# Kernel optimization log

Hardware: AMD Instinct MI355X
Metric: run time of the kernel (lower is better)

The kernel has to match this reference:

```python
import jax, jax.numpy as jnp
import numpy as np

EMBED_DIM = 1024
NUM_HEADS = 16
HEAD_DIM = EMBED_DIM // NUM_HEADS


def setup_inputs() -> dict:
    key = jax.random.key(0)
    ks = jax.random.split(key, 5)
    B, N, C = 2, 2048, EMBED_DIM
    s = 0.02
    return {
        "x": jax.random.normal(ks[0], (B, N, C), dtype=jnp.float32),
        "w_qkv": jax.random.normal(ks[1], (C, 3 * C), dtype=jnp.float32) * s,
        "b_qkv": jax.random.normal(ks[2], (3 * C,), dtype=jnp.float32) * s,
        "w_proj": jax.random.normal(ks[3], (C, C), dtype=jnp.float32) * s,
        "b_proj": jax.random.normal(ks[4], (C,), dtype=jnp.float32) * s,
    }


def reference(x, w_qkv, b_qkv, w_proj, b_proj):
    B, N, C = x.shape
    H, D = NUM_HEADS, C // NUM_HEADS
    scale = D ** -0.5
    qkv = x @ w_qkv + b_qkv                      # [B,N,3C]
    qkv = qkv.reshape(B, N, 3, H, D).transpose(2, 0, 3, 1, 4)  # [3,B,H,N,D]
    q, k, v = qkv[0] * scale, qkv[1], qkv[2]
    attn = jnp.einsum("bhnd,bhmd->bhnm", q, k)   # [B,H,N,N]
    attn = jax.nn.softmax(attn, axis=-1)
    out = jnp.einsum("bhnm,bhmd->bhnd", attn, v)  # [B,H,N,D]
    out = out.transpose(0, 2, 1, 3).reshape(B, N, C)
    return out @ w_proj + b_proj
```

## Files before the change

### kernel.cpp

```cpp
#include <hip/hip_runtime.h>

typedef short bf16x8 __attribute__((ext_vector_type(8)));
typedef float f32x4 __attribute__((ext_vector_type(4)));
typedef float f32x16 __attribute__((ext_vector_type(16)));
typedef unsigned short ushort8 __attribute__((ext_vector_type(8)));
typedef unsigned short ushort4v __attribute__((ext_vector_type(4)));
typedef unsigned int uint4v __attribute__((ext_vector_type(4)));
typedef unsigned short u16;

__device__ inline u16 f2bf(float f) {
  unsigned int u = __float_as_uint(f);
  u += 0x7fffu + ((u >> 16) & 1u);
  return (u16)(u >> 16);
}

__device__ inline unsigned cvt_pk_bf16(float lo, float hi2) {
  unsigned r;
  asm("v_cvt_pk_bf16_f32 %0, %1, %2" : "=v"(r) : "v"(lo), "v"(hi2));
  return r;
}

__device__ inline void perm32swap(unsigned& a, unsigned& b) {
  asm("v_permlane32_swap_b32 %0, %1" : "+v"(a), "+v"(b));
}

__device__ inline void gload_lds16(const u16* g, u16* l) {
  __builtin_amdgcn_global_load_lds(
      (const __attribute__((address_space(1))) unsigned int*)g,
      (__attribute__((address_space(3))) unsigned int*)l, 16, 0, 0);
}

__global__ __launch_bounds__(256) void cvt_bf16(const float* __restrict__ in,
                                                u16* __restrict__ out, int n) {
  int i = (blockIdx.x * 256 + threadIdx.x) * 8;
  if (i >= n) return;
  float4 a = *(const float4*)(in + i);
  float4 b = *(const float4*)(in + i + 4);
  ushort8 o;
  o[0] = f2bf(a.x); o[1] = f2bf(a.y); o[2] = f2bf(a.z); o[3] = f2bf(a.w);
  o[4] = f2bf(b.x); o[5] = f2bf(b.y); o[6] = f2bf(b.z); o[7] = f2bf(b.w);
  *(ushort8*)(out + i) = o;
}

__global__ __launch_bounds__(256) void trans_w(const float* __restrict__ W,
                                               u16* __restrict__ Wt, int K, int N) {
  const int k0 = blockIdx.x * 64, n0 = blockIdx.y * 64;
  const int tx = threadIdx.x & 63, ty = threadIdx.x >> 6;
  __shared__ float t[64][65];
#pragma unroll
  for (int i = 0; i < 16; ++i) {
    int r = i * 4 + ty;
    t[r][tx] = W[(size_t)(k0 + r) * N + n0 + tx];
  }
  __syncthreads();
#pragma unroll
  for (int i = 0; i < 16; ++i) {
    int r = i * 4 + ty;
    Wt[(size_t)(n0 + r) * K + k0 + tx] = f2bf(t[tx][r]);
  }
}

template <int MODE>
__global__ __launch_bounds__(256) void gemm_bt(
    const u16* __restrict__ A, const u16* __restrict__ Bt, int M, int N, int K,
    const float* __restrict__ bias, float* __restrict__ outF,
    u16* __restrict__ Qb, u16* __restrict__ Kb, u16* __restrict__ Vb) {
  const int bm = blockIdx.x * 128;
  const int bn = blockIdx.y * 128;
  const int tid = threadIdx.x;
  const int wid = tid >> 6;
  const int lr = tid & 15;
  const int lg = (tid >> 4) & 3;
  const int wr = wid >> 1, wc = wid & 1;

  __shared__ u16 smem[32768];
  u16* Ab0 = smem;
  u16* Ab1 = smem + 8192;
  u16* Bb0 = smem + 16384;
  u16* Bb1 = smem + 24576;

  f32x4 acc[4][4] = {};

  const int rowi = tid >> 3;
  const int sslot = ((tid & 7) ^ (rowi & 7)) * 8;
  const u16* Ag = A + (size_t)bm * K;
  const u16* Bg = Bt + (size_t)bn * K;
  const int nkt = K >> 6;

  auto stage = [&](u16* Ad, u16* Bd, int kt) {
    const int kof = kt << 6;
#pragma unroll
    for (int i = 0; i < 4; ++i) {
      const int row = i * 32 + rowi;
      gload_lds16(Ag + (size_t)row * K + kof + sslot, Ad + (i * 32 + wid * 8) * 64);
      gload_lds16(Bg + (size_t)row * K + kof + sslot, Bd + (i * 32 + wid * 8) * 64);
    }
  };

  stage(Ab0, Bb0, 0);
  __syncthreads();

  for (int kt = 0; kt < nkt; ++kt) {
    const int p = kt & 1;
    const char* Ard = (const char*)(p ? Ab1 : Ab0);
    const char* Brd = (const char*)(p ? Bb1 : Bb0);
    bf16x8 af[4], bfr[4];
#pragma unroll
    for (int t = 0; t < 4; ++t) {
      const int ra = wr * 64 + t * 16 + lr;
      const int rb = wc * 64 + t * 16 + lr;
      af[t] = *(const bf16x8*)(Ard + ra * 128 + ((lg * 16) ^ ((ra & 7) << 4)));
      bfr[t] = *(const bf16x8*)(Brd + rb * 128 + ((lg * 16) ^ ((rb & 7) << 4)));
    }
    if (kt + 1 < nkt) stage(p ? Ab0 : Ab1, p ? Bb0 : Bb1, kt + 1);
    __builtin_amdgcn_s_setprio(1);
#pragma unroll
    for (int mt = 0; mt < 4; ++mt)
#pragma unroll
      for (int nt = 0; nt < 4; ++nt)
        acc[mt][nt] = __builtin_amdgcn_mfma_f32_16x16x32_bf16(
            af[mt], bfr[nt], acc[mt][nt], 0, 0, 0);
    __builtin_amdgcn_s_setprio(0);
#pragma unroll
    for (int t = 0; t < 4; ++t) {
      const int ra = wr * 64 + t * 16 + lr;
      const int rb = wc * 64 + t * 16 + lr;
      af[t] = *(const bf16x8*)(Ard + ra * 128 + ((64 + lg * 16) ^ ((ra & 7) << 4)));
      bfr[t] = *(const bf16x8*)(Brd + rb * 128 + ((64 + lg * 16) ^ ((rb & 7) << 4)));
    }
    __builtin_amdgcn_s_setprio(1);
#pragma unroll
    for (int mt = 0; mt < 4; ++mt)
#pragma unroll
      for (int nt = 0; nt < 4; ++nt)
        acc[mt][nt] = __builtin_amdgcn_mfma_f32_16x16x32_bf16(
            af[mt], bfr[nt], acc[mt][nt], 0, 0, 0);
    __builtin_amdgcn_s_setprio(0);
    __syncthreads();
  }

  if (MODE == 1) {
#pragma unroll
    for (int mt = 0; mt < 4; ++mt) {
      const int row0 = bm + wr * 64 + mt * 16 + lg * 4;
#pragma unroll
      for (int nt = 0; nt < 4; ++nt) {
        const int col = bn + wc * 64 + nt * 16 + lr;
        const float bv = bias[col];
#pragma unroll
        for (int r = 0; r < 4; ++r)
          outF[(size_t)(row0 + r) * N + col] = acc[mt][nt][r] + bv;
      }
    }
    return;
  }

  u16* T = smem;
  const int which = bn >> 10;

  if (which == 2) {
#pragma unroll
    for (int nt = 0; nt < 4; ++nt) {
      const int cl = wc * 64 + nt * 16 + lr;
      const float bv = bias[bn + cl];
#pragma unroll
      for (int mt = 0; mt < 4; ++mt) {
        const int rlb = wr * 128 + mt * 32 + lg * 8;
        ushort4v pk;
#pragma unroll
        for (int r = 0; r < 4; ++r) pk[r] = f2bf(acc[mt][nt][r] + bv);
        *(ushort4v*)((char*)T + cl * 256 + (rlb ^ ((cl & 7) << 4))) = pk;
      }
    }
  } else {
    const float sc = (which == 0) ? 0.18033688f : 1.0f;
#pragma unroll
    for (int mt = 0; mt < 4; ++mt) {
      const int rl0 = wr * 64 + mt * 16 + lg * 4;
#pragma unroll
      for (int nt = 0; nt < 4; ++nt) {
        const int cl = wc * 64 + nt * 16 + lr;
        const float bv = bias[bn + cl];
#pragma unroll
        for (int r = 0; r < 4; ++r) {
          const int rl = rl0 + r;
          *(u16*)((char*)T + rl * 256 + ((cl * 2) ^ ((rl & 7) << 4))) =
              f2bf((acc[mt][nt][r] + bv) * sc);
        }
      }
    }
  }
  __syncthreads();

  const int b = bm >> 11;
  const int nbase = bm & 2047;
  if (which == 0) {
#pragma unroll
    for (int i = 0; i < 8; ++i) {
      const int c = i * 256 + tid;
      const int rl = c >> 4, dch = c & 15;
      uint4v v =
          *(const uint4v*)((const char*)T + rl * 256 + ((dch * 16) ^ ((rl & 7) << 4)));
      const int bh = b * 16 + (bn >> 6) + (dch >> 3);
      *(uint4v*)(Qb + ((size_t)bh * 2048 + nbase + rl) * 64 + (dch & 7) * 8) = v;
    }
  } else if (which == 1) {
#pragma unroll
    for (int i = 0; i < 8; ++i) {
      const int c = i * 256 + tid;
      const int lane = c & 63, s = (c >> 6) & 7, ktl = (c >> 9) & 1, hl = c >> 10;
      const int lq = lane & 31, hi2 = lane >> 5;
      const int rl = ktl * 64 + (s & 1) * 32 + lq;
      const int cc = hl * 128 + (s >> 1) * 32 + hi2 * 16;
      uint4v v = *(const uint4v*)((const char*)T + rl * 256 + (cc ^ ((rl & 7) << 4)));
      const int bh = b * 16 + ((bn & 1023) >> 6) + hl;
      const int kt2 = (nbase >> 6) + ktl;
      *(uint4v*)(Kb + ((((size_t)bh * 32 + kt2) * 8 + s) * 64 + lane) * 8) = v;
    }
  } else {
#pragma unroll
    for (int i = 0; i < 8; ++i) {
      const int c = i * 256 + tid;
      const int lane = c & 63, s = (c >> 6) & 7, ktl = (c >> 9) & 1, hl = c >> 10;
      const int lq = lane & 31, hi2 = lane >> 5;
      const int cl = hl * 64 + (s & 1) * 32 + lq;
      const int cc = ktl * 128 + (s >> 1) * 32 + hi2 * 16;
      uint4v v = *(const uint4v*)((const char*)T + cl * 256 + (cc ^ ((cl & 7) << 4)));
      const int bh = b * 16 + ((bn & 1023) >> 6) + hl;
      const int kt2 = (nbase >> 6) + ktl;
      *(uint4v*)(Vb + ((((size_t)bh * 32 + kt2) * 8 + s) * 64 + lane) * 8) = v;
    }
  }
}

__global__ __launch_bounds__(256, 2) void flash_attn12(const u16* __restrict__ Qb,
                                                       const u16* __restrict__ Kp,
                                                       const u16* __restrict__ Vp,
                                                       u16* __restrict__ AO) {
  const int bh = blockIdx.x & 31;
  const int qt = blockIdx.x >> 5;
  const int tid = threadIdx.x;
  const int w = tid >> 6;
  const int lane = tid & 63;
  const int lq = lane & 31;
  const int hi = lane >> 5;
  const int q0 = qt * 128 + w * 32;

  __shared__ u16 Kld[2][8192];
  __shared__ u16 Vld[2][8192];

  const u16* Qg = Qb + ((size_t)bh * 2048 + q0 + lq) * 64 + 8 * hi;
  bf16x8 qf[4];
#pragma unroll
  for (int t = 0; t < 4; ++t) qf[t] = *(const bf16x8*)(Qg + 16 * t);

  const u16* Kg = Kp + (size_t)bh * (32 * 4096);
  const u16* Vg = Vp + (size_t)bh * (32 * 4096);

  f32x16 ot0 = {}, ot1 = {};
  float lacc[8] = {};

  auto stage = [&](int p, int ph) {
    const size_t src = (size_t)ph * 8192;
#pragma unroll
    for (int j = 0; j < 4; ++j) {
      gload_lds16(Kg + src + j * 2048 + tid * 8, &Kld[p][j * 2048 + tid * 8]);
      gload_lds16(Vg + src + j * 2048 + tid * 8, &Vld[p][j * 2048 + tid * 8]);
    }
  };

  auto compute = [&](int p) {
    bf16x8 kf0[8], kf1[8];
#pragma unroll
    for (int s = 0; s < 8; ++s) {
      kf0[s] = *(const bf16x8*)&Kld[p][s * 512 + lane * 8];
      kf1[s] = *(const bf16x8*)&Kld[p][4096 + s * 512 + lane * 8];
    }

    f32x16 sa0 = {}, sb0 = {}, sa1 = {}, sb1 = {};
    __builtin_amdgcn_s_setprio(1);
#pragma unroll
    for (int t = 0; t < 4; ++t) {
      sa0 = __builtin_amdgcn_mfma_f32_32x32x16_bf16(kf0[2 * t], qf[t], sa0, 0, 0, 0);
      sb0 = __builtin_amdgcn_mfma_f32_32x32x16_bf16(kf0[2 * t + 1], qf[t], sb0, 0, 0, 0);
      sa1 = __builtin_amdgcn_mfma_f32_32x32x16_bf16(kf1[2 * t], qf[t], sa1, 0, 0, 0);
      sb1 = __builtin_amdgcn_mfma_f32_32x32x16_bf16(kf1[2 * t + 1], qf[t], sb1, 0, 0, 0);
    }
    __builtin_amdgcn_s_setprio(0);

    bf16x8 vf0[8];
#pragma unroll
    for (int s = 0; s < 8; ++s)
      vf0[s] = *(const bf16x8*)&Vld[p][s * 512 + lane * 8];

#pragma unroll
    for (int r = 0; r < 16; ++r) {
      sa0[r] = __builtin_amdgcn_exp2f(sa0[r]);
      sb0[r] = __builtin_amdgcn_exp2f(sb0[r]);
    }
#pragma unroll
    for (int r = 0; r < 8; ++r)
      lacc[r] += (sa0[r] + sa0[r + 8]) + (sb0[r] + sb0[r + 8]);

    unsigned Ua[8], Ub[8];
#pragma unroll
    for (int s = 0; s < 4; ++s)
#pragma unroll
      for (int m2 = 0; m2 < 2; ++m2) {
        Ua[s * 2 + m2] = cvt_pk_bf16(sa0[4 * s + 2 * m2], sa0[4 * s + 2 * m2 + 1]);
        Ub[s * 2 + m2] = cvt_pk_bf16(sb0[4 * s + 2 * m2], sb0[4 * s + 2 * m2 + 1]);
      }
    bf16x8 pfrag[4];
#pragma unroll
    for (int t = 0; t < 4; ++t) {
      const unsigned* U = (t < 2) ? Ua : Ub;
      const int tt = t & 1;
      unsigned w0 = U[(2 * tt) * 2 + 0], w2 = U[(2 * tt + 1) * 2 + 0];
      unsigned w1 = U[(2 * tt) * 2 + 1], w3 = U[(2 * tt + 1) * 2 + 1];
      perm32swap(w0, w2);
      perm32swap(w1, w3);
      uint4v uu = {w0, w1, w2, w3};
      pfrag[t] = __builtin_bit_cast(bf16x8, uu);
    }
    __builtin_amdgcn_s_setprio(1);
#pragma unroll
    for (int t = 0; t < 4; ++t) {
      ot0 = __builtin_amdgcn_mfma_f32_32x32x16_bf16(vf0[2 * t], pfrag[t], ot0, 0, 0, 0);
      ot1 = __builtin_amdgcn_mfma_f32_32x32x16_bf16(vf0[2 * t + 1], pfrag[t], ot1, 0, 0, 0);
    }
    __builtin_amdgcn_s_setprio(0);

    bf16x8 vf1[8];
#pragma unroll
    for (int s = 0; s < 8; ++s)
      vf1[s] = *(const bf16x8*)&Vld[p][4096 + s * 512 + lane * 8];

#pragma unroll
    for (int r = 0; r < 16; ++r) {
      sa1[r] = __builtin_amdgcn_exp2f(sa1[r]);
      sb1[r] = __builtin_amdgcn_exp2f(sb1[r]);
    }
#pragma unroll
    for (int r = 0; r < 8; ++r)
      lacc[r] += (sa1[r] + sa1[r + 8]) + (sb1[r] + sb1[r + 8]);

#pragma unroll
    for (int s = 0; s < 4; ++s)
#pragma unroll
      for (int m2 = 0; m2 < 2; ++m2) {
        Ua[s * 2 + m2] = cvt_pk_bf16(sa1[4 * s + 2 * m2], sa1[4 * s + 2 * m2 + 1]);
        Ub[s * 2 + m2] = cvt_pk_bf16(sb1[4 * s + 2 * m2], sb1[4 * s + 2 * m2 + 1]);
      }
#pragma unroll
    for (int t = 0; t < 4; ++t) {
      const unsigned* U = (t < 2) ? Ua : Ub;
      const int tt = t & 1;
      unsigned w0 = U[(2 * tt) * 2 + 0], w2 = U[(2 * tt + 1) * 2 + 0];
      unsigned w1 = U[(2 * tt) * 2 + 1], w3 = U[(2 * tt + 1) * 2 + 1];
      perm32swap(w0, w2);
      perm32swap(w1, w3);
      uint4v uu = {w0, w1, w2, w3};
      pfrag[t] = __builtin_bit_cast(bf16x8, uu);
    }
    __builtin_amdgcn_s_setprio(1);
#pragma unroll
    for (int t = 0; t < 4; ++t) {
      ot0 = __builtin_amdgcn_mfma_f32_32x32x16_bf16(vf1[2 * t], pfrag[t], ot0, 0, 0, 0);
      ot1 = __builtin_amdgcn_mfma_f32_32x32x16_bf16(vf1[2 * t + 1], pfrag[t], ot1, 0, 0, 0);
    }
    __builtin_amdgcn_s_setprio(0);
  };

  stage(0, 0);
  __syncthreads();

  for (int ph = 0; ph < 16; ++ph) {
    const int p = ph & 1;
    if (ph < 15) stage(p ^ 1, ph + 1);
    compute(p);
    __syncthreads();
  }

  float lsum = ((lacc[0] + lacc[1]) + (lacc[2] + lacc[3])) +
               ((lacc[4] + lacc[5]) + (lacc[6] + lacc[7]));
  lsum += __shfl_xor(lsum, 32, 64);
  const float inv = 1.0f / lsum;

  const int b = bh >> 4, h = bh & 15;
  u16* Ao = AO + ((size_t)(b * 2048 + q0 + lq)) * 1024 + h * 64;
#pragma unroll
  for (int s = 0; s < 4; ++s) {
    {
      const int d = 8 * s + 4 * hi;
      ushort4v pk;
#pragma unroll
      for (int i = 0; i < 4; ++i) pk[i] = f2bf(ot0[4 * s + i] * inv);
      *(ushort4v*)(Ao + d) = pk;
    }
    {
      const int d = 32 + 8 * s + 4 * hi;
      ushort4v pk;
#pragma unroll
      for (int i = 0; i < 4; ++i) pk[i] = f2bf(ot1[4 * s + i] * inv);
      *(ushort4v*)(Ao + d) = pk;
    }
  }
}

extern "C" void kernel_launch(void* const* d_in, const int* in_sizes, int n_in,
                              void* d_out, int out_size, void* d_ws, size_t ws_size,
                              hipStream_t stream) {
  const float* x = (const float*)d_in[0];
  const float* w_qkv = (const float*)d_in[1];
  const float* b_qkv = (const float*)d_in[2];
  const float* w_proj = (const float*)d_in[3];
  const float* b_proj = (const float*)d_in[4];
  float* out = (float*)d_out;

  char* ws = (char*)d_ws;
  u16* xb = (u16*)(ws);
  u16* wqT = (u16*)(ws + (8ull << 20));
  u16* wpT = (u16*)(ws + (14ull << 20));
  u16* Qb = (u16*)(ws + (16ull << 20));
  u16* Kp = (u16*)(ws + (24ull << 20));
  u16* Vp = (u16*)(ws + (32ull << 20));
  u16* AO = (u16*)(ws + (40ull << 20));

  cvt_bf16<<<dim3(2048), dim3(256), 0, stream>>>(x, xb, 4194304);
  trans_w<<<dim3(16, 48), dim3(256), 0, stream>>>(w_qkv, wqT, 1024, 3072);
  trans_w<<<dim3(16, 16), dim3(256), 0, stream>>>(w_proj, wpT, 1024, 1024);
  gemm_bt<0><<<dim3(32, 24), dim3(256), 0, stream>>>(xb, wqT, 4096, 3072, 1024,
                                                     b_qkv, nullptr, Qb, Kp, Vp);
  flash_attn12<<<dim3(512), dim3(256), 0, stream>>>(Qb, Kp, Vp, AO);
  gemm_bt<1><<<dim3(32, 8), dim3(256), 0, stream>>>(AO, wpT, 4096, 1024, 1024,
                                                    b_proj, out, nullptr, nullptr,
                                                    nullptr);
}
```

Before: 108.9 us.

## Use 256x256 tiles with 512 threads and swizzled block order for QKV GEMM

Replaces the templated 128x128 QKV GEMM with a dedicated kernel that computes 256x256 output tiles using 8 waves and 128 KB of LDS. Block indices are remapped so neighbouring blocks share A and B panels in cache. The goal is more reuse per loaded tile and fewer blocks, 192 instead of 768. The cost is one block per CU, which on a 256-CU part leaves some CUs idle, plus heavy register and LDS pressure that limits latency hiding.

```diff
diff --git a/kernel.cpp b/kernel.cpp
--- a/kernel.cpp
+++ b/kernel.cpp
@@ -60,11 +60,176 @@
   }
 }
 
-template <int MODE>
-__global__ __launch_bounds__(256) void gemm_bt(
+__global__ __launch_bounds__(512, 1) void gemm256_qkv(
+    const u16* __restrict__ A, const u16* __restrict__ Bt,
+    const float* __restrict__ bias, u16* __restrict__ Qb,
+    u16* __restrict__ Kb, u16* __restrict__ Vb) {
+  const int K = 1024;
+  const int lid = blockIdx.x;
+  const int swz = (lid & 7) * 24 + (lid >> 3);
+  const int bm = (swz & 15) * 256;
+  const int bn = (swz >> 4) * 256;
+
+  const int tid = threadIdx.x;
+  const int wid = tid >> 6;
+  const int lane = tid & 63;
+  const int lr = lane & 15;
+  const int lg = (lane >> 4) & 3;
+  const int wr = wid >> 2;
+  const int wc = wid & 3;
+
+  __shared__ u16 smem[65536];
+  u16* Ab0 = smem;
+  u16* Ab1 = smem + 16384;
+  u16* Bb0 = smem + 32768;
+  u16* Bb1 = smem + 49152;
+
+  f32x4 acc[8][4] = {};
+
+  const int rowi = tid >> 3;
+  const int sslot = ((tid & 7) ^ (rowi & 7)) * 8;
+  const u16* Ag = A + (size_t)bm * K;
+  const u16* Bg = Bt + (size_t)bn * K;
+
+  auto stage = [&](u16* Ad, u16* Bd, int kt) {
+    const int kof = kt << 6;
+#pragma unroll
+    for (int i = 0; i < 4; ++i) {
+      const int row = i * 64 + rowi;
+      gload_lds16(Ag + (size_t)row * K + kof + sslot, Ad + (i * 64 + wid * 8) * 64);
+      gload_lds16(Bg + (size_t)row * K + kof + sslot, Bd + (i * 64 + wid * 8) * 64);
+    }
+  };
+
+  stage(Ab0, Bb0, 0);
+  __syncthreads();
+
+  for (int kt = 0; kt < 16; ++kt) {
+    const int p = kt & 1;
+    const char* Ard = (const char*)(p ? Ab1 : Ab0);
+    const char* Brd = (const char*)(p ? Bb1 : Bb0);
+    bf16x8 af[8], bfr[4];
+#pragma unroll
+    for (int t = 0; t < 8; ++t) {
+      const int ra = wr * 128 + t * 16 + lr;
+      af[t] = *(const bf16x8*)(Ard + ra * 128 + ((lg * 16) ^ ((ra & 7) << 4)));
+    }
+#pragma unroll
+    for (int t = 0; t < 4; ++t) {
+      const int rb = wc * 64 + t * 16 + lr;
+      bfr[t] = *(const bf16x8*)(Brd + rb * 128 + ((lg * 16) ^ ((rb & 7) << 4)));
+    }
+    if (kt + 1 < 16) stage(p ? Ab0 : Ab1, p ? Bb0 : Bb1, kt + 1);
+    __builtin_amdgcn_s_setprio(1);
+#pragma unroll
+    for (int mt = 0; mt < 8; ++mt)
+#pragma unroll
+      for (int nt = 0; nt < 4; ++nt)
+        acc[mt][nt] = __builtin_amdgcn_mfma_f32_16x16x32_bf16(
+            af[mt], bfr[nt], acc[mt][nt], 0, 0, 0);
+    __builtin_amdgcn_s_setprio(0);
+#pragma unroll
+    for (int t = 0; t < 8; ++t) {
+      const int ra = wr * 128 + t * 16 + lr;
+      af[t] = *(const bf16x8*)(Ard + ra * 128 + ((64 + lg * 16) ^ ((ra & 7) << 4)));
+    }
+#pragma unroll
+    for (int t = 0; t < 4; ++t) {
+      const int rb = wc * 64 + t * 16 + lr;
+      bfr[t] = *(const bf16x8*)(Brd + rb * 128 + ((64 + lg * 16) ^ ((rb & 7) << 4)));
+    }
+    __builtin_amdgcn_s_setprio(1);
+#pragma unroll
+    for (int mt = 0; mt < 8; ++mt)
+#pragma unroll
+      for (int nt = 0; nt < 4; ++nt)
+        acc[mt][nt] = __builtin_amdgcn_mfma_f32_16x16x32_bf16(
+            af[mt], bfr[nt], acc[mt][nt], 0, 0, 0);
+    __builtin_amdgcn_s_setprio(0);
+    __syncthreads();
+  }
+
+  u16* T = smem;
+  const int which = bn >> 10;
+
+  if (which == 2) {
+#pragma unroll
+    for (int nt = 0; nt < 4; ++nt) {
+      const int cl = wc * 64 + nt * 16 + lr;
+      const float bv = bias[bn + cl];
+#pragma unroll
+      for (int mt = 0; mt < 8; ++mt) {
+        const int rlb = wr * 256 + mt * 32 + lg * 8;
+        ushort4v pk;
+#pragma unroll
+        for (int r = 0; r < 4; ++r) pk[r] = f2bf(acc[mt][nt][r] + bv);
+        *(ushort4v*)((char*)T + cl * 512 + (rlb ^ ((cl & 7) << 4))) = pk;
+      }
+    }
+  } else {
+    const float sc = (which == 0) ? 0.18033688f : 1.0f;
+#pragma unroll
+    for (int mt = 0; mt < 8; ++mt) {
+      const int rl0 = wr * 128 + mt * 16 + lg * 4;
+#pragma unroll
+      for (int nt = 0; nt < 4; ++nt) {
+        const int cl = wc * 64 + nt * 16 + lr;
+        const float bv = bias[bn + cl];
+#pragma unroll
+        for (int r = 0; r < 4; ++r) {
+          const int rl = rl0 + r;
+          *(u16*)((char*)T + rl * 512 + ((cl * 2) ^ ((rl & 7) << 4))) =
+              f2bf((acc[mt][nt][r] + bv) * sc);
+        }
+      }
+    }
+  }
+  __syncthreads();
+
+  const int b = bm >> 11;
+  const int nbase = bm & 2047;
+  if (which == 0) {
+#pragma unroll
+    for (int i = 0; i < 16; ++i) {
+      const int c = i * 512 + tid;
+      const int rl = c >> 5, dch = c & 31;
+      uint4v v =
+          *(const uint4v*)((const char*)T + rl * 512 + ((dch * 16) ^ ((rl & 7) << 4)));
+      const int bh = b * 16 + (bn >> 6) + (dch >> 3);
+      *(uint4v*)(Qb + ((size_t)bh * 2048 + nbase + rl) * 64 + (dch & 7) * 8) = v;
+    }
+  } else if (which == 1) {
+#pragma unroll
+    for (int i = 0; i < 16; ++i) {
+      const int c = i * 512 + tid;
+      const int ln = c & 63, s = (c >> 6) & 7, ktl = (c >> 9) & 3, hl = (c >> 11) & 3;
+      const int lq = ln & 31, hi2 = ln >> 5;
+      const int rl = ktl * 64 + (s & 1) * 32 + lq;
+      const int cc = hl * 128 + (s >> 1) * 32 + hi2 * 16;
+      uint4v v = *(const uint4v*)((const char*)T + rl * 512 + (cc ^ ((rl & 7) << 4)));
+      const int bh = b * 16 + ((bn & 1023) >> 6) + hl;
+      const int kt2 = (nbase >> 6) + ktl;
+      *(uint4v*)(Kb + ((((size_t)bh * 32 + kt2) * 8 + s) * 64 + ln) * 8) = v;
+    }
+  } else {
+#pragma unroll
+    for (int i = 0; i < 16; ++i) {
+      const int c = i * 512 + tid;
+      const int ln = c & 63, s = (c >> 6) & 7, ktl = (c >> 9) & 3, hl = (c >> 11) & 3;
+      const int lq = ln & 31, hi2 = ln >> 5;
+      const int cl = hl * 64 + (s & 1) * 32 + lq;
+      const int cc = ktl * 128 + (s >> 1) * 32 + hi2 * 16;
+      uint4v v = *(const uint4v*)((const char*)T + cl * 512 + (cc ^ ((cl & 7) << 4)));
+      const int bh = b * 16 + ((bn & 1023) >> 6) + hl;
+      const int kt2 = (nbase >> 6) + ktl;
+      *(uint4v*)(Vb + ((((size_t)bh * 32 + kt2) * 8 + s) * 64 + ln) * 8) = v;
+    }
+  }
+}
+
+__global__ __launch_bounds__(256) void gemm_proj(
     const u16* __restrict__ A, const u16* __restrict__ Bt, int M, int N, int K,
-    const float* __restrict__ bias, float* __restrict__ outF,
-    u16* __restrict__ Qb, u16* __restrict__ Kb, u16* __restrict__ Vb) {
+    const float* __restrict__ bias, float* __restrict__ outF) {
   const int bm = blockIdx.x * 128;
   const int bn = blockIdx.y * 128;
   const int tid = threadIdx.x;
@@ -139,96 +304,16 @@
     __syncthreads();
   }
 
-  if (MODE == 1) {
-#pragma unroll
-    for (int mt = 0; mt < 4; ++mt) {
-      const int row0 = bm + wr * 64 + mt * 16 + lg * 4;
-#pragma unroll
-      for (int nt = 0; nt < 4; ++nt) {
-        const int col = bn + wc * 64 + nt * 16 + lr;
-        const float bv = bias[col];
-#pragma unroll
-        for (int r = 0; r < 4; ++r)
-          outF[(size_t)(row0 + r) * N + col] = acc[mt][nt][r] + bv;
-      }
-    }
-    return;
-  }
-
-  u16* T = smem;
-  const int which = bn >> 10;
-
-  if (which == 2) {
+#pragma unroll
+  for (int mt = 0; mt < 4; ++mt) {
+    const int row0 = bm + wr * 64 + mt * 16 + lg * 4;
 #pragma unroll
     for (int nt = 0; nt < 4; ++nt) {
-      const int cl = wc * 64 + nt * 16 + lr;
-      const float bv = bias[bn + cl];
-#pragma unroll
-      for (int mt = 0; mt < 4; ++mt) {
-        const int rlb = wr * 128 + mt * 32 + lg * 8;
-        ushort4v pk;
-#pragma unroll
-        for (int r = 0; r < 4; ++r) pk[r] = f2bf(acc[mt][nt][r] + bv);
-        *(ushort4v*)((char*)T + cl * 256 + (rlb ^ ((cl & 7) << 4))) = pk;
-      }
-    }
-  } else {
-    const float sc = (which == 0) ? 0.18033688f : 1.0f;
-#pragma unroll
-    for (int mt = 0; mt < 4; ++mt) {
-      const int rl0 = wr * 64 + mt * 16 + lg * 4;
-#pragma unroll
-      for (int nt = 0; nt < 4; ++nt) {
-        const int cl = wc * 64 + nt * 16 + lr;
-        const float bv = bias[bn + cl];
-#pragma unroll
-        for (int r = 0; r < 4; ++r) {
-          const int rl = rl0 + r;
-          *(u16*)((char*)T + rl * 256 + ((cl * 2) ^ ((rl & 7) << 4))) =
-              f2bf((acc[mt][nt][r] + bv) * sc);
-        }
-      }
-    }
-  }
-  __syncthreads();
-
-  const int b = bm >> 11;
-  const int nbase = bm & 2047;
-  if (which == 0) {
-#pragma unroll
-    for (int i = 0; i < 8; ++i) {
-      const int c = i * 256 + tid;
-      const int rl = c >> 4, dch = c & 15;
-      uint4v v =
-          *(const uint4v*)((const char*)T + rl * 256 + ((dch * 16) ^ ((rl & 7) << 4)));
-      const int bh = b * 16 + (bn >> 6) + (dch >> 3);
-      *(uint4v*)(Qb + ((size_t)bh * 2048 + nbase + rl) * 64 + (dch & 7) * 8) = v;
-    }
-  } else if (which == 1) {
-#pragma unroll
-    for (int i = 0; i < 8; ++i) {
-      const int c = i * 256 + tid;
-      const int lane = c & 63, s = (c >> 6) & 7, ktl = (c >> 9) & 1, hl = c >> 10;
-      const int lq = lane & 31, hi2 = lane >> 5;
-      const int rl = ktl * 64 + (s & 1) * 32 + lq;
-      const int cc = hl * 128 + (s >> 1) * 32 + hi2 * 16;
-      uint4v v = *(const uint4v*)((const char*)T + rl * 256 + (cc ^ ((rl & 7) << 4)));
-      const int bh = b * 16 + ((bn & 1023) >> 6) + hl;
-      const int kt2 = (nbase >> 6) + ktl;
-      *(uint4v*)(Kb + ((((size_t)bh * 32 + kt2) * 8 + s) * 64 + lane) * 8) = v;
-    }
-  } else {
-#pragma unroll
-    for (int i = 0; i < 8; ++i) {
-      const int c = i * 256 + tid;
-      const int lane = c & 63, s = (c >> 6) & 7, ktl = (c >> 9) & 1, hl = c >> 10;
-      const int lq = lane & 31, hi2 = lane >> 5;
-      const int cl = hl * 64 + (s & 1) * 32 + lq;
-      const int cc = ktl * 128 + (s >> 1) * 32 + hi2 * 16;
-      uint4v v = *(const uint4v*)((const char*)T + cl * 256 + (cc ^ ((cl & 7) << 4)));
-      const int bh = b * 16 + ((bn & 1023) >> 6) + hl;
-      const int kt2 = (nbase >> 6) + ktl;
-      *(uint4v*)(Vb + ((((size_t)bh * 32 + kt2) * 8 + s) * 64 + lane) * 8) = v;
+      const int col = bn + wc * 64 + nt * 16 + lr;
+      const float bv = bias[col];
+#pragma unroll
+      for (int r = 0; r < 4; ++r)
+        outF[(size_t)(row0 + r) * N + col] = acc[mt][nt][r] + bv;
     }
   }
 }
@@ -429,10 +514,8 @@
   cvt_bf16<<<dim3(2048), dim3(256), 0, stream>>>(x, xb, 4194304);
   trans_w<<<dim3(16, 48), dim3(256), 0, stream>>>(w_qkv, wqT, 1024, 3072);
   trans_w<<<dim3(16, 16), dim3(256), 0, stream>>>(w_proj, wpT, 1024, 1024);
-  gemm_bt<0><<<dim3(32, 24), dim3(256), 0, stream>>>(xb, wqT, 4096, 3072, 1024,
-                                                     b_qkv, nullptr, Qb, Kp, Vp);
+  gemm256_qkv<<<dim3(192), dim3(512), 0, stream>>>(xb, wqT, b_qkv, Qb, Kp, Vp);
   flash_attn12<<<dim3(512), dim3(256), 0, stream>>>(Qb, Kp, Vp, AO);
-  gemm_bt<1><<<dim3(32, 8), dim3(256), 0, stream>>>(AO, wpT, 4096, 1024, 1024,
-                                                    b_proj, out, nullptr, nullptr,
-                                                    nullptr);
-}
+  gemm_proj<<<dim3(32, 8), dim3(256), 0, stream>>>(AO, wpT, 4096, 1024, 1024,
+                                                   b_proj, out);
+}
```

Result: no change. 107.5 us (-1.4%).
